# Kernel tuning notes

Hardware: AMD Instinct MI355X
Metric: run time of the kernel (lower is better)

Reference implementation:

```python
import jax, jax.numpy as jnp
import numpy as np

N_SRC = 65536   # layer-0 (source) nodes
N_DST = 2048    # layer-1 (destination) nodes = first N_DST parents
DEG = 32        # uniform in-degree -> dense mailbox [N_DST, DEG]
E = N_DST * DEG
T = 16          # edge temporal sequence length
D_EDGE = 16     # edge_in_dim
D_NODE = 128    # node_in_dim
H = 128         # node_hidden_dim
N_CLASS = 10


def _tlstm(e, dt, e_len, W, U, b, Wd, bd):
    """Time-aware LSTM (T-LSTM) over per-edge sequences.
    e: [E,T,D_EDGE], dt: [E,T], e_len: [E] int. Returns h at step e_len-1: [E,H].
    Cell-memory decomposition: c_s = tanh(c Wd + bd); c* = (c - c_s) + c_s * g(dt),
    g(dt) = 1/log(e + dt); then standard LSTM gate update."""
    n = e.shape[0]
    x_proj = jnp.einsum('etd,dk->etk', e, W) + b           # [E,T,4H]
    decay = 1.0 / jnp.log(jnp.float32(np.e) + dt)          # [E,T]

    def step(carry, inp):
        h, c = carry
        xp, dec = inp                                      # [E,4H], [E]
        c_s = jnp.tanh(c @ Wd + bd)
        c_star = (c - c_s) + c_s * dec[:, None]
        gates = xp + h @ U
        i, f, o, g = jnp.split(gates, 4, axis=-1)
        c_new = jax.nn.sigmoid(f) * c_star + jax.nn.sigmoid(i) * jnp.tanh(g)
        h_new = jax.nn.sigmoid(o) * jnp.tanh(c_new)
        return (h_new, c_new), h_new

    init = (jnp.zeros((n, H), e.dtype), jnp.zeros((n, H), e.dtype))
    _, hs = jax.lax.scan(step, init, (jnp.swapaxes(x_proj, 0, 1), jnp.swapaxes(decay, 0, 1)))
    hs = jnp.swapaxes(hs, 0, 1)                            # [E,T,H]
    idx = jnp.clip(e_len - 1, 0, T - 1)
    return jnp.take_along_axis(hs, idx[:, None, None], axis=1)[:, 0, :]


def _sparsemax(z):
    """Sparsemax along last axis (faithful to the torch sort/cumsum version)."""
    K = z.shape[-1]
    z = z - jnp.max(z, axis=-1, keepdims=True)
    zs = -jnp.sort(-z, axis=-1)                            # descending sort
    rng = jnp.arange(1, K + 1, dtype=z.dtype)
    bound = 1.0 + rng * zs
    cum = jnp.cumsum(zs, axis=-1)
    is_gt = (bound > cum).astype(z.dtype)
    k = jnp.max(is_gt * rng, axis=-1, keepdims=True)
    taus = (jnp.sum(is_gt * zs, axis=-1, keepdims=True) - 1.0) / k
    return jnp.maximum(0.0, z - taus)


def _forward(node_features, e, delta_t,
             tlstm_m_W, tlstm_m_U, tlstm_m_b, tlstm_m_Wd, tlstm_m_bd,
             tlstm_a_W, tlstm_a_U, tlstm_a_b, tlstm_a_Wd, tlstm_a_bd,
             attn_w, edge_out_W, edge_out_b, node_W, node_b, fc_W, fc_b,
             e_len, src_idx):
    h0 = node_features                                     # layer-0 activation
    self_h = h0[:N_DST]                                    # dst nodes mapped into layer 0
    self_h_tmp = jnp.concatenate([self_h, jnp.zeros((N_DST, H), h0.dtype)], axis=1) @ edge_out_W + edge_out_b
    # --- message_func over all edges ---
    h_src = h0[src_idx]                                    # gather [E, D_NODE]
    e_out = _tlstm(e, delta_t, e_len, tlstm_m_W, tlstm_m_U, tlstm_m_b, tlstm_m_Wd, tlstm_m_bd)
    a_h = _tlstm(e, delta_t, e_len, tlstm_a_W, tlstm_a_U, tlstm_a_b, tlstm_a_Wd, tlstm_a_bd)
    a = jax.nn.leaky_relu((a_h @ attn_w)[:, 0])            # [E]
    m = jax.nn.relu(jnp.concatenate([h_src, e_out], axis=1) @ edge_out_W + edge_out_b)  # [E,H]
    # --- reduce_func: sparsemax attention + sum over mailbox ---
    alpha = _sparsemax(a.reshape(N_DST, DEG))
    h_agg = jnp.einsum('nd,ndh->nh', alpha, m.reshape(N_DST, DEG, H))
    # --- NodeUpdate ---
    h_agg = h_agg - self_h_tmp
    act = jax.nn.relu(jnp.concatenate([self_h, h_agg], axis=1) @ node_W + node_b)
    return act @ fc_W + fc_b                               # [N_DST, N_CLASS]


def setup_inputs():
    key = jax.random.key(0)
    ks = jax.random.split(key, 24)
    s = 0.05
    return {
        "node_features": jax.random.normal(ks[0], (N_SRC, D_NODE), jnp.float32),
        "e": jax.random.normal(ks[1], (E, T, D_EDGE), jnp.float32),
        "delta_t": jax.random.uniform(ks[2], (E, T), jnp.float32, 0.0, 10.0),
        "tlstm_m_W": jax.random.normal(ks[3], (D_EDGE, 4 * H), jnp.float32) * s,
        "tlstm_m_U": jax.random.normal(ks[4], (H, 4 * H), jnp.float32) * s,
        "tlstm_m_b": jnp.zeros((4 * H,), jnp.float32),
        "tlstm_m_Wd": jax.random.normal(ks[5], (H, H), jnp.float32) * s,
        "tlstm_m_bd": jnp.zeros((H,), jnp.float32),
        "tlstm_a_W": jax.random.normal(ks[6], (D_EDGE, 4 * H), jnp.float32) * s,
        "tlstm_a_U": jax.random.normal(ks[7], (H, 4 * H), jnp.float32) * s,
        "tlstm_a_b": jnp.zeros((4 * H,), jnp.float32),
        "tlstm_a_Wd": jax.random.normal(ks[8], (H, H), jnp.float32) * s,
        "tlstm_a_bd": jnp.zeros((H,), jnp.float32),
        "attn_w": jax.random.normal(ks[9], (H, 1), jnp.float32) * s,
        "edge_out_W": jax.random.normal(ks[10], (D_NODE + H, H), jnp.float32) * s,
        "edge_out_b": jnp.zeros((H,), jnp.float32),
        "node_W": jax.random.normal(ks[11], (D_NODE + H, H), jnp.float32) * s,
        "node_b": jnp.zeros((H,), jnp.float32),
        "fc_W": jax.random.normal(ks[12], (H, N_CLASS), jnp.float32) * s,
        "fc_b": jnp.zeros((N_CLASS,), jnp.float32),
        "e_len": jax.random.randint(ks[13], (E,), 1, T + 1).astype(jnp.int32),
        "src_idx": jax.random.randint(ks[14], (E,), 0, N_SRC).astype(jnp.int32),
    }


def reference(node_features, e, delta_t,
              tlstm_m_W, tlstm_m_U, tlstm_m_b, tlstm_m_Wd, tlstm_m_bd,
              tlstm_a_W, tlstm_a_U, tlstm_a_b, tlstm_a_Wd, tlstm_a_bd,
              attn_w, edge_out_W, edge_out_b, node_W, node_b, fc_W, fc_b,
              e_len, src_idx):
    return _forward(node_features, e, delta_t,
                    tlstm_m_W, tlstm_m_U, tlstm_m_b, tlstm_m_Wd, tlstm_m_bd,
                    tlstm_a_W, tlstm_a_U, tlstm_a_b, tlstm_a_Wd, tlstm_a_bd,
                    attn_w, edge_out_W, edge_out_b, node_W, node_b, fc_W, fc_b,
                    e_len, src_idx)
```

## Files before the change

### kernel.cpp

```cpp
#include <hip/hip_runtime.h>


typedef unsigned short u16;
typedef unsigned int u32;
typedef unsigned long long u64;
typedef float f32x4 __attribute__((ext_vector_type(4)));
typedef short bf16x8 __attribute__((ext_vector_type(8)));

#define NDST 2048
#define EDGES 65536

__device__ __forceinline__ float bf2f(u16 u) {
  union { u32 i; float f; } v; v.i = ((u32)u) << 16; return v.f;
}
__device__ __forceinline__ u16 f2bf(float f) {
  u32 x = __builtin_bit_cast(u32, f);
  u32 r = x + 0x7fffu + ((x >> 16) & 1u);
  return (u16)(r >> 16);
}
__device__ __forceinline__ u32 cvtpk2(float lo, float hi) {
  u32 r;
  asm("v_cvt_pk_bf16_f32 %0, %1, %2" : "=v"(r) : "v"(lo), "v"(hi));
  return r;
}
__device__ __forceinline__ u16 f2bf_h(float f) { return (u16)(cvtpk2(f, f) & 0xffffu); }
__device__ __forceinline__ bf16x8 ldb8(const u16* p) {
  return *reinterpret_cast<const bf16x8*>(p);
}
__device__ __forceinline__ f32x4 mfma16(bf16x8 a, bf16x8 b, f32x4 c) {
  return __builtin_amdgcn_mfma_f32_16x16x32_bf16(a, b, c, 0, 0, 0);
}
__device__ __forceinline__ float rcp_(float x) { return __builtin_amdgcn_rcpf(x); }
__device__ __forceinline__ float sigm(float x) { return rcp_(1.f + __expf(-x)); }
__device__ __forceinline__ float tanh_(float x) { return 2.f * rcp_(1.f + __expf(-2.f * x)) - 1.f; }

__global__ __launch_bounds__(256) void prep_kernel(
    const float* __restrict__ U_m, const float* __restrict__ W_m,
    const float* __restrict__ U_a, const float* __restrict__ W_a,
    const float* __restrict__ Wd_m, const float* __restrict__ Wd_a,
    const float* __restrict__ eoW, const float* __restrict__ ndW,
    const float* __restrict__ fcW,
    u16* __restrict__ UWt_m, u16* __restrict__ UWt_a,
    u16* __restrict__ WdT_m, u16* __restrict__ WdT_a, u16* __restrict__ eoWt,
    u16* __restrict__ ndWt, u16* __restrict__ fcWt)
{
  int idx = blockIdx.x * 256 + threadIdx.x;
  if (idx < 163840) {
    int s = idx >= 81920 ? 1 : 0;
    int i = idx - s * 81920;
    int j = i / 160, k = i % 160;
    const float* U = s ? U_a : U_m;
    const float* W = s ? W_a : W_m;
    float v = 0.f;
    if (k < 128) v = U[k * 512 + j];
    else if (k < 144) v = W[(k - 128) * 512 + j];
    (s ? UWt_a : UWt_m)[j * 160 + k] = f2bf(v);
  } else if (idx < 196608) {
    int i = idx - 163840;
    int s = i >= 16384 ? 1 : 0;
    i -= s * 16384;
    int j = i >> 7, k = i & 127;
    (s ? WdT_a : WdT_m)[j * 128 + k] = f2bf((s ? Wd_a : Wd_m)[k * 128 + j]);
  } else if (idx < 229376) {
    int i = idx - 196608;
    int j = i >> 8, k = i & 255;
    eoWt[j * 256 + k] = f2bf(eoW[k * 128 + j]);
  } else if (idx < 262144) {
    int i = idx - 229376;
    int j = i >> 8, k = i & 255;
    ndWt[j * 256 + k] = f2bf(ndW[k * 128 + j]);
  } else if (idx < 264192) {
    int i = idx - 262144;
    int j = i >> 7, k = i & 127;
    fcWt[j * 128 + k] = (j < 10) ? f2bf(fcW[k * 10 + j]) : (u16)0;
  }
}

__global__ __launch_bounds__(256) void hist_kernel(const int* __restrict__ elen,
                                                   int* __restrict__ cnt) {
  __shared__ int wcnt[4][16];
  const int tid = threadIdx.x;
  const int e = blockIdx.x * 256 + tid;
  const int wv = tid >> 6, ln = tid & 63;
  const int b = min(max(elen[e] - 1, 0), 15);
#pragma unroll
  for (int bb = 0; bb < 16; ++bb) {
    u64 m = __ballot(b == bb);
    if (ln == 0) wcnt[wv][bb] = __popcll(m);
  }
  __syncthreads();
  if (tid < 16)
    atomicAdd(&cnt[tid], wcnt[0][tid] + wcnt[1][tid] + wcnt[2][tid] + wcnt[3][tid]);
}
__global__ void scan_kernel(const int* __restrict__ cnt, int* __restrict__ coff) {
  if (threadIdx.x == 0 && blockIdx.x == 0) {
    int a = 0;
    for (int i = 0; i < 16; ++i) { coff[i] = a; a += cnt[i]; }
  }
}
__global__ __launch_bounds__(256) void scatter_kernel(const int* __restrict__ elen,
                                                      int* __restrict__ coff,
                                                      int* __restrict__ perm) {
  __shared__ int wcnt[4][16];
  __shared__ int base[16];
  const int tid = threadIdx.x;
  const int e = blockIdx.x * 256 + tid;
  const int wv = tid >> 6, ln = tid & 63;
  const int b = min(max(elen[e] - 1, 0), 15);
  int intrarank = 0;
#pragma unroll
  for (int bb = 0; bb < 16; ++bb) {
    u64 m = __ballot(b == bb);
    if (bb == b) intrarank = __popcll(m & ((1ull << ln) - 1ull));
    if (ln == 0) wcnt[wv][bb] = __popcll(m);
  }
  __syncthreads();
  if (tid < 16) {
    int s = wcnt[0][tid] + wcnt[1][tid] + wcnt[2][tid] + wcnt[3][tid];
    base[tid] = atomicAdd(&coff[tid], s);
  }
  __syncthreads();
  int prior = 0;
  for (int w = 0; w < wv; ++w) prior += wcnt[w][b];
  perm[base[b] + prior + intrarank] = e;
}

__global__ __launch_bounds__(256) void pre_gemm(
    const float* __restrict__ nf, const float* __restrict__ eob,
    const u16* __restrict__ eoWt, float* __restrict__ sft)
{
  const int n0 = blockIdx.x * 32;
  const int tid = threadIdx.x;
  const int w = tid >> 6, lane = tid & 63, l15 = lane & 15, lhi = lane >> 4;
  __shared__ __align__(16) u16 A3[32 * 136];

  {
    const int row = tid >> 3, p = tid & 7;
    const float4* ph = reinterpret_cast<const float4*>(nf + (size_t)(n0 + row) * 128 + p * 16);
    float4 f0 = ph[0], f1 = ph[1], f2 = ph[2], f3 = ph[3];
    uint4 pk0, pk1;
    pk0.x = cvtpk2(f0.x, f0.y); pk0.y = cvtpk2(f0.z, f0.w);
    pk0.z = cvtpk2(f1.x, f1.y); pk0.w = cvtpk2(f1.z, f1.w);
    pk1.x = cvtpk2(f2.x, f2.y); pk1.y = cvtpk2(f2.z, f2.w);
    pk1.z = cvtpk2(f3.x, f3.y); pk1.w = cvtpk2(f3.z, f3.w);
    *reinterpret_cast<uint4*>(&A3[row * 136 + p * 16]) = pk0;
    *reinterpret_cast<uint4*>(&A3[row * 136 + p * 16 + 8]) = pk1;
  }
  __syncthreads();
  f32x4 acc[2][2];
  const int j0 = w * 32 + l15, j1 = w * 32 + 16 + l15;
  {
    float v0 = eob[j0], v1 = eob[j1];
    f32x4 t0 = {v0, v0, v0, v0}, t1 = {v1, v1, v1, v1};
    acc[0][0] = t0; acc[1][0] = t0;
    acc[0][1] = t1; acc[1][1] = t1;
  }
#pragma unroll
  for (int ks = 0; ks < 4; ++ks) {
    bf16x8 a0 = ldb8(&A3[l15 * 136 + ks * 32 + lhi * 8]);
    bf16x8 a1 = ldb8(&A3[(16 + l15) * 136 + ks * 32 + lhi * 8]);
    bf16x8 b0 = ldb8(eoWt + (size_t)j0 * 256 + ks * 32 + lhi * 8);
    bf16x8 b1 = ldb8(eoWt + (size_t)j1 * 256 + ks * 32 + lhi * 8);
    acc[0][0] = mfma16(a0, b0, acc[0][0]);
    acc[1][0] = mfma16(a1, b0, acc[1][0]);
    acc[0][1] = mfma16(a0, b1, acc[0][1]);
    acc[1][1] = mfma16(a1, b1, acc[1][1]);
  }
#pragma unroll
  for (int m = 0; m < 2; ++m)
#pragma unroll
    for (int n = 0; n < 2; ++n)
#pragma unroll
      for (int r = 0; r < 4; ++r) {
        const int row = m * 16 + lhi * 4 + r;
        const int j = w * 32 + n * 16 + l15;
        sft[(size_t)(n0 + row) * 128 + j] = acc[m][n][r];
      }
}

__global__ __launch_bounds__(512, 2)
void lstm_kernel(
    const float* __restrict__ e, const float* __restrict__ dtt,
    const float* __restrict__ b_m, const float* __restrict__ bd_m,
    const float* __restrict__ b_a, const float* __restrict__ bd_a,
    const float* __restrict__ attn,
    const int* __restrict__ elen, const int* __restrict__ perm,
    const u16* __restrict__ UWt_m, const u16* __restrict__ UWt_a,
    const u16* __restrict__ WdT_m, const u16* __restrict__ WdT_a,
    u16* __restrict__ e_out, float* __restrict__ aval_g)
{
  const int bid = blockIdx.x;
  const int sel = bid >> 11;
  const int edge0 = (2047 - (bid & 2047)) * 32;
  const u16* UWt = sel ? UWt_a : UWt_m;
  const u16* WdT = sel ? WdT_a : WdT_m;
  const float* bg  = sel ? b_a  : b_m;
  const float* bdp = sel ? bd_a : bd_m;

  __shared__ __align__(16) u16 Abuf[2][32 * 168];
  __shared__ __align__(16) u16 Cbuf[2][32 * 136];
  __shared__ __align__(16) u16 Eo[32 * 136];
  __shared__ float dec_all[16][32];
  __shared__ int rowedge[32], elen_s[32], tmax_s;

  const int tid = threadIdx.x;
  const int ww = tid >> 6, lane = tid & 63, l15 = lane & 15, lhi = lane >> 4;
  const int j = ww * 16 + l15;
  const int srow = tid >> 3, sp = tid & 7;

  if (tid < 32) {
    int ed = perm[edge0 + tid];
    rowedge[tid] = ed;
    elen_s[tid] = min(max(elen[ed], 1), 16);
  }
  for (int i = tid; i < 2 * 32 * 168; i += 512) (&Abuf[0][0])[i] = 0;
  for (int i = tid; i < 2 * 32 * 136; i += 512) (&Cbuf[0][0])[i] = 0;
  __syncthreads();
  if (tid == 0) {
    int mx = 1;
    for (int i = 0; i < 32; ++i) mx = max(mx, elen_s[i]);
    tmax_s = mx;
  }
  {
    int row = tid & 31, t = tid >> 5;
    dec_all[t][row] =
        1.f / logf(2.7182818284590452f + dtt[(size_t)rowedge[row] * 16 + t]);
  }
  if (tid < 256) {
    float2 e2 = *reinterpret_cast<const float2*>(e + (size_t)rowedge[srow] * 256 + sp * 2);
    *reinterpret_cast<u32*>(&Abuf[0][srow * 168 + 128 + sp * 2]) = cvtpk2(e2.x, e2.y);
  }

  bf16x8 BU[5][4];
#pragma unroll
  for (int ks = 0; ks < 5; ++ks)
#pragma unroll
    for (int g = 0; g < 4; ++g)
      BU[ks][g] = ldb8(UWt + (size_t)(g * 128 + j) * 160 + ks * 32 + lhi * 8);
  bf16x8 BD[4];
#pragma unroll
  for (int ks = 0; ks < 4; ++ks)
    BD[ks] = ldb8(WdT + (size_t)j * 128 + ks * 32 + lhi * 8);
#pragma unroll
  for (int ks = 0; ks < 5; ++ks)
#pragma unroll
    for (int g = 0; g < 4; ++g)
      asm volatile("" : "+v"(BU[ks][g]));
#pragma unroll
  for (int ks = 0; ks < 4; ++ks)
    asm volatile("" : "+v"(BD[ks]));

  f32x4 bias4[4];
#pragma unroll
  for (int g = 0; g < 4; ++g) {
    float b = bg[g * 128 + j];
    f32x4 t = {b, b, b, b};
    bias4[g] = t;
  }
  f32x4 bds4;
  {
    float b = bdp[j];
    f32x4 t = {b, b, b, b};
    bds4 = t;
  }

  float cst[2][4];
#pragma unroll
  for (int m = 0; m < 2; ++m)
#pragma unroll
    for (int r = 0; r < 4; ++r) cst[m][r] = 0.f;
  __syncthreads();
  const int tmax = tmax_s;

  for (int t = 0; t < tmax; ++t) {
    const u16* Ar = Abuf[t & 1];
    const u16* Cr = Cbuf[t & 1];
    u16* Aw = Abuf[(t + 1) & 1];
    u16* Cw = Cbuf[(t + 1) & 1];

    f32x4 acc[2][4];
    f32x4 accs[2];
    {
      bf16x8 a0 = ldb8(&Ar[l15 * 168 + lhi * 8]);
      bf16x8 a1 = ldb8(&Ar[(16 + l15) * 168 + lhi * 8]);
#pragma unroll
      for (int g = 0; g < 4; ++g) {
        acc[0][g] = mfma16(a0, BU[0][g], bias4[g]);
        acc[1][g] = mfma16(a1, BU[0][g], bias4[g]);
      }
    }
#pragma unroll
    for (int ks = 1; ks < 5; ++ks) {
      bf16x8 a0 = ldb8(&Ar[l15 * 168 + ks * 32 + lhi * 8]);
      bf16x8 a1 = ldb8(&Ar[(16 + l15) * 168 + ks * 32 + lhi * 8]);
#pragma unroll
      for (int g = 0; g < 4; ++g) {
        acc[0][g] = mfma16(a0, BU[ks][g], acc[0][g]);
        acc[1][g] = mfma16(a1, BU[ks][g], acc[1][g]);
      }
    }
    {
      bf16x8 c0 = ldb8(&Cr[l15 * 136 + lhi * 8]);
      bf16x8 c1 = ldb8(&Cr[(16 + l15) * 136 + lhi * 8]);
      accs[0] = mfma16(c0, BD[0], bds4);
      accs[1] = mfma16(c1, BD[0], bds4);
    }
#pragma unroll
    for (int ks = 1; ks < 4; ++ks) {
      bf16x8 c0 = ldb8(&Cr[l15 * 136 + ks * 32 + lhi * 8]);
      bf16x8 c1 = ldb8(&Cr[(16 + l15) * 136 + ks * 32 + lhi * 8]);
      accs[0] = mfma16(c0, BD[ks], accs[0]);
      accs[1] = mfma16(c1, BD[ks], accs[1]);
    }

    float2 e2n;
    const bool stage_next = (t + 1 < tmax);
    if (stage_next && tid < 256)
      e2n = *reinterpret_cast<const float2*>(
          e + (size_t)rowedge[srow] * 256 + (t + 1) * 16 + sp * 2);

#pragma unroll
    for (int m = 0; m < 2; ++m)
#pragma unroll
      for (int r = 0; r < 4; ++r) {
        const int row = m * 16 + lhi * 4 + r;
        float iv = sigm(acc[m][0][r]);
        float fv = sigm(acc[m][1][r]);
        float ov = sigm(acc[m][2][r]);
        float gv = tanh_(acc[m][3][r]);
        float cs = tanh_(accs[m][r]);
        float dec = dec_all[t][row];
        float co = cst[m][r];
        float cstar = co + cs * (dec - 1.f);
        float cn = fv * cstar + iv * gv;
        float hn = ov * tanh_(cn);
        cst[m][r] = cn;
        u16 hb = f2bf_h(hn);
        Aw[row * 168 + j] = hb;
        Cw[row * 136 + j] = f2bf_h(cn);
        if (elen_s[row] == t + 1) Eo[row * 136 + j] = hb;
      }
    if (stage_next && tid < 256)
      *reinterpret_cast<u32*>(&Aw[srow * 168 + 128 + sp * 2]) = cvtpk2(e2n.x, e2n.y);
    __syncthreads();
  }

  if (sel) {
    if (tid < 32) {
      float s = 0.f;
      for (int k = 0; k < 128; ++k) s += bf2f(Eo[tid * 136 + k]) * attn[k];
      aval_g[rowedge[tid]] = s > 0.f ? s : 0.01f * s;
    }
  } else if (tid < 256) {
    uint4 v0 = *reinterpret_cast<const uint4*>(&Eo[srow * 136 + sp * 16]);
    uint4 v1 = *reinterpret_cast<const uint4*>(&Eo[srow * 136 + sp * 16 + 8]);
    u16* dst = e_out + (size_t)rowedge[srow] * 128 + sp * 16;
    *reinterpret_cast<uint4*>(dst) = v0;
    *reinterpret_cast<uint4*>(dst + 8) = v1;
  }
}

__global__ __launch_bounds__(256) void node_mid(
    const float* __restrict__ nf, const u16* __restrict__ e_out,
    const float* __restrict__ aval_g, const float* __restrict__ eob,
    const int* __restrict__ srci, const u16* __restrict__ eoWt,
    const float* __restrict__ sft, u16* __restrict__ haggb)
{
  const int node = blockIdx.x;
  const int tid = threadIdx.x;
  const int ebase = node * 32;
  const int w = tid >> 6, lane = tid & 63, l15 = lane & 15, lhi = lane >> 4;

  __shared__ __align__(16) u16 A2[32 * 264];
  __shared__ __align__(16) u16 Msh[32 * 136];
  __shared__ float aval[32], zsrc[32], zs[32], redf[32], alpha_s[32];
  __shared__ int redi[32];

  {
    const int row = tid >> 3, p = tid & 7;
    const int src = srci[ebase + row];
    const float4* ph = reinterpret_cast<const float4*>(nf + (size_t)src * 128 + p * 16);
    float4 f0 = ph[0], f1 = ph[1], f2 = ph[2], f3 = ph[3];
    uint4 pk0, pk1;
    pk0.x = cvtpk2(f0.x, f0.y); pk0.y = cvtpk2(f0.z, f0.w);
    pk0.z = cvtpk2(f1.x, f1.y); pk0.w = cvtpk2(f1.z, f1.w);
    pk1.x = cvtpk2(f2.x, f2.y); pk1.y = cvtpk2(f2.z, f2.w);
    pk1.z = cvtpk2(f3.x, f3.y); pk1.w = cvtpk2(f3.z, f3.w);
    *reinterpret_cast<uint4*>(&A2[row * 264 + p * 16]) = pk0;
    *reinterpret_cast<uint4*>(&A2[row * 264 + p * 16 + 8]) = pk1;
    const u16* pe = e_out + (size_t)(ebase + row) * 128 + p * 16;
    *reinterpret_cast<uint4*>(&A2[row * 264 + 128 + p * 16]) =
        *reinterpret_cast<const uint4*>(pe);
    *reinterpret_cast<uint4*>(&A2[row * 264 + 128 + p * 16 + 8]) =
        *reinterpret_cast<const uint4*>(pe + 8);
  }
  if (tid < 32) aval[tid] = aval_g[ebase + tid];
  __syncthreads();

  {
    f32x4 eacc[2][2];
    const int j0 = w * 32 + l15, j1 = w * 32 + 16 + l15;
    {
      float v0 = eob[j0], v1 = eob[j1];
      f32x4 t0 = {v0, v0, v0, v0}, t1 = {v1, v1, v1, v1};
      eacc[0][0] = t0; eacc[1][0] = t0;
      eacc[0][1] = t1; eacc[1][1] = t1;
    }
#pragma unroll
    for (int ks = 0; ks < 8; ++ks) {
      bf16x8 a0 = ldb8(&A2[l15 * 264 + ks * 32 + lhi * 8]);
      bf16x8 a1 = ldb8(&A2[(16 + l15) * 264 + ks * 32 + lhi * 8]);
      bf16x8 b0 = ldb8(eoWt + (size_t)j0 * 256 + ks * 32 + lhi * 8);
      bf16x8 b1 = ldb8(eoWt + (size_t)j1 * 256 + ks * 32 + lhi * 8);
      eacc[0][0] = mfma16(a0, b0, eacc[0][0]);
      eacc[1][0] = mfma16(a1, b0, eacc[1][0]);
      eacc[0][1] = mfma16(a0, b1, eacc[0][1]);
      eacc[1][1] = mfma16(a1, b1, eacc[1][1]);
    }
#pragma unroll
    for (int m = 0; m < 2; ++m)
#pragma unroll
      for (int n = 0; n < 2; ++n)
#pragma unroll
        for (int r = 0; r < 4; ++r) {
          const int row = m * 16 + lhi * 4 + r;
          const int jj = w * 32 + n * 16 + l15;
          Msh[row * 136 + jj] = f2bf_h(fmaxf(eacc[m][n][r], 0.f));
        }
  }
  __syncthreads();

  if (tid < 32) {
    float mx = -1e30f;
    for (int jj = 0; jj < 32; ++jj) mx = fmaxf(mx, aval[jj]);
    float z = aval[tid] - mx;
    zsrc[tid] = z;
    int rank = 0;
    for (int jj = 0; jj < 32; ++jj) {
      float zj = aval[jj] - mx;
      rank += (zj > z) || (zj == z && jj < tid);
    }
    zs[rank] = z;
  }
  __syncthreads();
  if (tid < 32) {
    float cum = 0.f;
    for (int s = 0; s <= tid; ++s) cum += zs[s];
    float zst = zs[tid];
    bool isg = (1.f + (float)(tid + 1) * zst) > cum;
    redf[tid] = isg ? zst : 0.f;
    redi[tid] = isg ? (tid + 1) : 0;
  }
  __syncthreads();
  if (tid < 32) {
    int kk = 0; float ss = 0.f;
    for (int jj = 0; jj < 32; ++jj) { kk = max(kk, redi[jj]); ss += redf[jj]; }
    float tau = (ss - 1.f) / (float)kk;
    alpha_s[tid] = fmaxf(0.f, zsrc[tid] - tau);
  }
  __syncthreads();

  if (tid < 128) {
    float s = 0.f;
    for (int d = 0; d < 32; ++d) s += alpha_s[d] * bf2f(Msh[d * 136 + tid]);
    haggb[(size_t)node * 128 + tid] = f2bf_h(s - sft[(size_t)node * 128 + tid]);
  }
}

__global__ __launch_bounds__(256) void post_gemm(
    const float* __restrict__ nf, const u16* __restrict__ haggb,
    const float* __restrict__ ndb, const u16* __restrict__ ndWt,
    const float* __restrict__ fcb, const u16* __restrict__ fcWt,
    float* __restrict__ out)
{
  const int n0 = blockIdx.x * 32;
  const int tid = threadIdx.x;
  const int w = tid >> 6, lane = tid & 63, l15 = lane & 15, lhi = lane >> 4;
  __shared__ __align__(16) u16 A3[32 * 264];
  __shared__ __align__(16) u16 Acts[32 * 136];

  {
    const int row = tid >> 3, p = tid & 7;
    const float4* ph = reinterpret_cast<const float4*>(nf + (size_t)(n0 + row) * 128 + p * 16);
    float4 f0 = ph[0], f1 = ph[1], f2 = ph[2], f3 = ph[3];
    uint4 pk0, pk1;
    pk0.x = cvtpk2(f0.x, f0.y); pk0.y = cvtpk2(f0.z, f0.w);
    pk0.z = cvtpk2(f1.x, f1.y); pk0.w = cvtpk2(f1.z, f1.w);
    pk1.x = cvtpk2(f2.x, f2.y); pk1.y = cvtpk2(f2.z, f2.w);
    pk1.z = cvtpk2(f3.x, f3.y); pk1.w = cvtpk2(f3.z, f3.w);
    *reinterpret_cast<uint4*>(&A3[row * 264 + p * 16]) = pk0;
    *reinterpret_cast<uint4*>(&A3[row * 264 + p * 16 + 8]) = pk1;
    const u16* pg = haggb + (size_t)(n0 + row) * 128 + p * 16;
    *reinterpret_cast<uint4*>(&A3[row * 264 + 128 + p * 16]) =
        *reinterpret_cast<const uint4*>(pg);
    *reinterpret_cast<uint4*>(&A3[row * 264 + 128 + p * 16 + 8]) =
        *reinterpret_cast<const uint4*>(pg + 8);
  }
  __syncthreads();

  {
    f32x4 acc[2][2];
    const int j0 = w * 32 + l15, j1 = w * 32 + 16 + l15;
    {
      float v0 = ndb[j0], v1 = ndb[j1];
      f32x4 t0 = {v0, v0, v0, v0}, t1 = {v1, v1, v1, v1};
      acc[0][0] = t0; acc[1][0] = t0;
      acc[0][1] = t1; acc[1][1] = t1;
    }
#pragma unroll
    for (int ks = 0; ks < 8; ++ks) {
      bf16x8 a0 = ldb8(&A3[l15 * 264 + ks * 32 + lhi * 8]);
      bf16x8 a1 = ldb8(&A3[(16 + l15) * 264 + ks * 32 + lhi * 8]);
      bf16x8 b0 = ldb8(ndWt + (size_t)j0 * 256 + ks * 32 + lhi * 8);
      bf16x8 b1 = ldb8(ndWt + (size_t)j1 * 256 + ks * 32 + lhi * 8);
      acc[0][0] = mfma16(a0, b0, acc[0][0]);
      acc[1][0] = mfma16(a1, b0, acc[1][0]);
      acc[0][1] = mfma16(a0, b1, acc[0][1]);
      acc[1][1] = mfma16(a1, b1, acc[1][1]);
    }
#pragma unroll
    for (int m = 0; m < 2; ++m)
#pragma unroll
      for (int n = 0; n < 2; ++n)
#pragma unroll
        for (int r = 0; r < 4; ++r) {
          const int row = m * 16 + lhi * 4 + r;
          const int jj = w * 32 + n * 16 + l15;
          Acts[row * 136 + jj] = f2bf_h(fmaxf(acc[m][n][r], 0.f));
        }
  }
  __syncthreads();

  if (w < 2) {
    const int m = w;
    f32x4 acc1;
    {
      float v = (l15 < 10) ? fcb[l15] : 0.f;
      f32x4 t = {v, v, v, v};
      acc1 = t;
    }
#pragma unroll
    for (int ks = 0; ks < 4; ++ks) {
      bf16x8 a = ldb8(&Acts[(m * 16 + l15) * 136 + ks * 32 + lhi * 8]);
      bf16x8 b = ldb8(fcWt + (size_t)l15 * 128 + ks * 32 + lhi * 8);
      acc1 = mfma16(a, b, acc1);
    }
    if (l15 < 10) {
#pragma unroll
      for (int r = 0; r < 4; ++r) {
        const int row = m * 16 + lhi * 4 + r;
        out[(size_t)(n0 + row) * 10 + l15] = acc1[r];
      }
    }
  }
}

extern "C" void kernel_launch(void* const* d_in, const int* in_sizes, int n_in,
                              void* d_out, int out_size, void* d_ws, size_t ws_size,
                              hipStream_t stream)
{
  const float* nf   = (const float*)d_in[0];
  const float* e    = (const float*)d_in[1];
  const float* dtt  = (const float*)d_in[2];
  const float* W_m  = (const float*)d_in[3];
  const float* U_m  = (const float*)d_in[4];
  const float* b_m  = (const float*)d_in[5];
  const float* Wd_m = (const float*)d_in[6];
  const float* bd_m = (const float*)d_in[7];
  const float* W_a  = (const float*)d_in[8];
  const float* U_a  = (const float*)d_in[9];
  const float* b_a  = (const float*)d_in[10];
  const float* Wd_a = (const float*)d_in[11];
  const float* bd_a = (const float*)d_in[12];
  const float* attn = (const float*)d_in[13];
  const float* eoW  = (const float*)d_in[14];
  const float* eob  = (const float*)d_in[15];
  const float* ndW  = (const float*)d_in[16];
  const float* ndb  = (const float*)d_in[17];
  const float* fcW  = (const float*)d_in[18];
  const float* fcb  = (const float*)d_in[19];
  const int* elen = (const int*)d_in[20];
  const int* srci = (const int*)d_in[21];

  char* ws = (char*)d_ws;
  u16* UWt_m  = (u16*)(ws + 0);
  u16* UWt_a  = (u16*)(ws + 163840);
  u16* WdT_m  = (u16*)(ws + 327680);
  u16* WdT_a  = (u16*)(ws + 360448);
  u16* eoWt   = (u16*)(ws + 393216);
  u16* e_out  = (u16*)(ws + 458752);
  float* aval = (float*)(ws + 17235968);
  int* perm   = (int*)(ws + 17498112);
  int* cnt    = (int*)(ws + 17760256);
  int* coff   = (int*)(ws + 17760320);
  u16* ndWt   = (u16*)(ws + 17760384);
  u16* fcWt   = (u16*)(ws + 17825920);
  float* sft  = (float*)(ws + 17830016);
  u16* haggb  = (u16*)(ws + 18878592);

  hipMemsetAsync(cnt, 0, 64, stream);
  prep_kernel<<<1032, 256, 0, stream>>>(U_m, W_m, U_a, W_a, Wd_m, Wd_a, eoW, ndW, fcW,
                                        UWt_m, UWt_a, WdT_m, WdT_a, eoWt, ndWt, fcWt);
  hist_kernel<<<EDGES / 256, 256, 0, stream>>>(elen, cnt);
  scan_kernel<<<1, 1, 0, stream>>>(cnt, coff);
  scatter_kernel<<<EDGES / 256, 256, 0, stream>>>(elen, coff, perm);
  pre_gemm<<<NDST / 32, 256, 0, stream>>>(nf, eob, eoWt, sft);
  lstm_kernel<<<4096, 512, 0, stream>>>(e, dtt, b_m, bd_m, b_a, bd_a, attn,
                                        elen, perm, UWt_m, UWt_a, WdT_m, WdT_a,
                                        e_out, aval);
  node_mid<<<NDST, 256, 0, stream>>>(nf, e_out, aval, eob, srci, eoWt, sft, haggb);
  post_gemm<<<NDST / 32, 256, 0, stream>>>(nf, haggb, ndb, ndWt, fcb, fcWt,
                                           (float*)d_out);
}
```

Measured before the change: 511.9 us.

## Process 64 edges per LSTM block instead of 32 to amortize weight loads

Each LSTM block now handles 64 edge rows (four 16-row MFMA tiles) rather than 32, and the grid is halved to 2048 blocks. Each wave's register-resident U/Wd weight fragments are reused across twice as many rows, and the per-step barrier and weight-preload costs are spread over more work. In exchange, accumulator registers and LDS roughly double, which may reduce occupancy under launch_bounds(512,2). Per-block tmax is the max over 64 sorted edges, so some padded timesteps may be added.

After: 496.9 us. -2.9%, faster.

```diff
diff --git a/kernel.cpp b/kernel.cpp
--- a/kernel.cpp
+++ b/kernel.cpp
@@ -190,43 +190,43 @@
     u16* __restrict__ e_out, float* __restrict__ aval_g)
 {
   const int bid = blockIdx.x;
-  const int sel = bid >> 11;
-  const int edge0 = (2047 - (bid & 2047)) * 32;
+  const int sel = bid >> 10;
+  const int edge0 = (1023 - (bid & 1023)) * 64;
   const u16* UWt = sel ? UWt_a : UWt_m;
   const u16* WdT = sel ? WdT_a : WdT_m;
   const float* bg  = sel ? b_a  : b_m;
   const float* bdp = sel ? bd_a : bd_m;
 
-  __shared__ __align__(16) u16 Abuf[2][32 * 168];
-  __shared__ __align__(16) u16 Cbuf[2][32 * 136];
-  __shared__ __align__(16) u16 Eo[32 * 136];
-  __shared__ float dec_all[16][32];
-  __shared__ int rowedge[32], elen_s[32], tmax_s;
+  __shared__ __align__(16) u16 Abuf[2][64 * 168];
+  __shared__ __align__(16) u16 Cbuf[2][64 * 136];
+  __shared__ __align__(16) u16 Eo[64 * 136];
+  __shared__ float dec_all[16][64];
+  __shared__ int rowedge[64], elen_s[64], tmax_s;
 
   const int tid = threadIdx.x;
   const int ww = tid >> 6, lane = tid & 63, l15 = lane & 15, lhi = lane >> 4;
   const int j = ww * 16 + l15;
   const int srow = tid >> 3, sp = tid & 7;
 
-  if (tid < 32) {
+  if (tid < 64) {
     int ed = perm[edge0 + tid];
     rowedge[tid] = ed;
     elen_s[tid] = min(max(elen[ed], 1), 16);
   }
-  for (int i = tid; i < 2 * 32 * 168; i += 512) (&Abuf[0][0])[i] = 0;
-  for (int i = tid; i < 2 * 32 * 136; i += 512) (&Cbuf[0][0])[i] = 0;
+  for (int i = tid; i < 2 * 64 * 168; i += 512) (&Abuf[0][0])[i] = 0;
+  for (int i = tid; i < 2 * 64 * 136; i += 512) (&Cbuf[0][0])[i] = 0;
   __syncthreads();
   if (tid == 0) {
     int mx = 1;
-    for (int i = 0; i < 32; ++i) mx = max(mx, elen_s[i]);
+    for (int i = 0; i < 64; ++i) mx = max(mx, elen_s[i]);
     tmax_s = mx;
   }
-  {
-    int row = tid & 31, t = tid >> 5;
+  for (int i = tid; i < 1024; i += 512) {
+    int row = i & 63, t = i >> 6;
     dec_all[t][row] =
         1.f / logf(2.7182818284590452f + dtt[(size_t)rowedge[row] * 16 + t]);
   }
-  if (tid < 256) {
+  {
     float2 e2 = *reinterpret_cast<const float2*>(e + (size_t)rowedge[srow] * 256 + sp * 2);
     *reinterpret_cast<u32*>(&Abuf[0][srow * 168 + 128 + sp * 2]) = cvtpk2(e2.x, e2.y);
   }
@@ -264,11 +264,11 @@
     bds4 = t;
   }
 
-  float cst[2][4];
-#pragma unroll
-  for (int m = 0; m < 2; ++m)
-#pragma unroll
-    for (int r = 0; r < 4; ++r) cst[m][r] = 0.f;
+  float cst[4][4];
+#pragma unroll
+  for (int mt = 0; mt < 4; ++mt)
+#pragma unroll
+    for (int r = 0; r < 4; ++r) cst[mt][r] = 0.f;
   __syncthreads();
   const int tmax = tmax_s;
 
@@ -278,80 +278,82 @@
     u16* Aw = Abuf[(t + 1) & 1];
     u16* Cw = Cbuf[(t + 1) & 1];
 
-    f32x4 acc[2][4];
-    f32x4 accs[2];
+    f32x4 acc[4][4];
+    f32x4 accs[4];
     {
-      bf16x8 a0 = ldb8(&Ar[l15 * 168 + lhi * 8]);
-      bf16x8 a1 = ldb8(&Ar[(16 + l15) * 168 + lhi * 8]);
-#pragma unroll
-      for (int g = 0; g < 4; ++g) {
-        acc[0][g] = mfma16(a0, BU[0][g], bias4[g]);
-        acc[1][g] = mfma16(a1, BU[0][g], bias4[g]);
+#pragma unroll
+      for (int mt = 0; mt < 4; ++mt) {
+        bf16x8 a = ldb8(&Ar[(mt * 16 + l15) * 168 + lhi * 8]);
+#pragma unroll
+        for (int g = 0; g < 4; ++g)
+          acc[mt][g] = mfma16(a, BU[0][g], bias4[g]);
       }
     }
 #pragma unroll
     for (int ks = 1; ks < 5; ++ks) {
-      bf16x8 a0 = ldb8(&Ar[l15 * 168 + ks * 32 + lhi * 8]);
-      bf16x8 a1 = ldb8(&Ar[(16 + l15) * 168 + ks * 32 + lhi * 8]);
-#pragma unroll
-      for (int g = 0; g < 4; ++g) {
-        acc[0][g] = mfma16(a0, BU[ks][g], acc[0][g]);
-        acc[1][g] = mfma16(a1, BU[ks][g], acc[1][g]);
+#pragma unroll
+      for (int mt = 0; mt < 4; ++mt) {
+        bf16x8 a = ldb8(&Ar[(mt * 16 + l15) * 168 + ks * 32 + lhi * 8]);
+#pragma unroll
+        for (int g = 0; g < 4; ++g)
+          acc[mt][g] = mfma16(a, BU[ks][g], acc[mt][g]);
       }
     }
     {
-      bf16x8 c0 = ldb8(&Cr[l15 * 136 + lhi * 8]);
-      bf16x8 c1 = ldb8(&Cr[(16 + l15) * 136 + lhi * 8]);
-      accs[0] = mfma16(c0, BD[0], bds4);
-      accs[1] = mfma16(c1, BD[0], bds4);
+#pragma unroll
+      for (int mt = 0; mt < 4; ++mt) {
+        bf16x8 c = ldb8(&Cr[(mt * 16 + l15) * 136 + lhi * 8]);
+        accs[mt] = mfma16(c, BD[0], bds4);
+      }
     }
 #pragma unroll
     for (int ks = 1; ks < 4; ++ks) {
-      bf16x8 c0 = ldb8(&Cr[l15 * 136 + ks * 32 + lhi * 8]);
-      bf16x8 c1 = ldb8(&Cr[(16 + l15) * 136 + ks * 32 + lhi * 8]);
-      accs[0] = mfma16(c0, BD[ks], accs[0]);
-      accs[1] = mfma16(c1, BD[ks], accs[1]);
+#pragma unroll
+      for (int mt = 0; mt < 4; ++mt) {
+        bf16x8 c = ldb8(&Cr[(mt * 16 + l15) * 136 + ks * 32 + lhi * 8]);
+        accs[mt] = mfma16(c, BD[ks], accs[mt]);
+      }
     }
 
     float2 e2n;
     const bool stage_next = (t + 1 < tmax);
-    if (stage_next && tid < 256)
+    if (stage_next)
       e2n = *reinterpret_cast<const float2*>(
           e + (size_t)rowedge[srow] * 256 + (t + 1) * 16 + sp * 2);
 
 #pragma unroll
-    for (int m = 0; m < 2; ++m)
+    for (int mt = 0; mt < 4; ++mt)
 #pragma unroll
       for (int r = 0; r < 4; ++r) {
-        const int row = m * 16 + lhi * 4 + r;
-        float iv = sigm(acc[m][0][r]);
-        float fv = sigm(acc[m][1][r]);
-        float ov = sigm(acc[m][2][r]);
-        float gv = tanh_(acc[m][3][r]);
-        float cs = tanh_(accs[m][r]);
+        const int row = mt * 16 + lhi * 4 + r;
+        float iv = sigm(acc[mt][0][r]);
+        float fv = sigm(acc[mt][1][r]);
+        float ov = sigm(acc[mt][2][r]);
+        float gv = tanh_(acc[mt][3][r]);
+        float cs = tanh_(accs[mt][r]);
         float dec = dec_all[t][row];
-        float co = cst[m][r];
+        float co = cst[mt][r];
         float cstar = co + cs * (dec - 1.f);
         float cn = fv * cstar + iv * gv;
         float hn = ov * tanh_(cn);
-        cst[m][r] = cn;
+        cst[mt][r] = cn;
         u16 hb = f2bf_h(hn);
         Aw[row * 168 + j] = hb;
         Cw[row * 136 + j] = f2bf_h(cn);
         if (elen_s[row] == t + 1) Eo[row * 136 + j] = hb;
       }
-    if (stage_next && tid < 256)
+    if (stage_next)
       *reinterpret_cast<u32*>(&Aw[srow * 168 + 128 + sp * 2]) = cvtpk2(e2n.x, e2n.y);
     __syncthreads();
   }
 
   if (sel) {
-    if (tid < 32) {
+    if (tid < 64) {
       float s = 0.f;
       for (int k = 0; k < 128; ++k) s += bf2f(Eo[tid * 136 + k]) * attn[k];
       aval_g[rowedge[tid]] = s > 0.f ? s : 0.01f * s;
     }
-  } else if (tid < 256) {
+  } else {
     uint4 v0 = *reinterpret_cast<const uint4*>(&Eo[srow * 136 + sp * 16]);
     uint4 v1 = *reinterpret_cast<const uint4*>(&Eo[srow * 136 + sp * 16 + 8]);
     u16* dst = e_out + (size_t)rowedge[srow] * 128 + sp * 16;
@@ -605,7 +607,7 @@
   scan_kernel<<<1, 1, 0, stream>>>(cnt, coff);
   scatter_kernel<<<EDGES / 256, 256, 0, stream>>>(elen, coff, perm);
   pre_gemm<<<NDST / 32, 256, 0, stream>>>(nf, eob, eoWt, sft);
-  lstm_kernel<<<4096, 512, 0, stream>>>(e, dtt, b_m, bd_m, b_a, bd_a, attn,
+  lstm_kernel<<<2048, 512, 0, stream>>>(e, dtt, b_m, bd_m, b_a, bd_a, attn,
                                         elen, perm, UWt_m, UWt_a, WdT_m, WdT_a,
                                         e_out, aval);
   node_mid<<<NDST, 256, 0, stream>>>(nf, e_out, aval, eob, srci, eoWt, sft, haggb);
```
